# Kernel optimization log

Measured on AMD Instinct MI355X. Metric: run time of the kernel, lower is better.

## Reference

```python
import jax, jax.numpy as jnp
import numpy as np
import math

B, S, E = 4, 2048, 1024

def setup_inputs() -> dict:
    key = jax.random.key(0)
    ks = jax.random.split(key, 12)
    scale = 1.0 / math.sqrt(E)
    inp = {
        "query": jax.random.normal(ks[0], (B, S, E), jnp.float32),
        "key_": jax.random.normal(ks[1], (B, S, E), jnp.float32),
        "value": jax.random.normal(ks[2], (B, S, E), jnp.float32),
        # causal mask, broadcast over batch: 1 = keep, 0 = mask
        "mask": jnp.broadcast_to(jnp.tril(jnp.ones((S, S), jnp.int32)), (B, S, S)),
        "Wq": jax.random.uniform(ks[3], (E, E), jnp.float32, -scale, scale),
        "bq": jax.random.uniform(ks[4], (E,), jnp.float32, -scale, scale),
        "Wk": jax.random.uniform(ks[5], (E, E), jnp.float32, -scale, scale),
        "bk": jax.random.uniform(ks[6], (E,), jnp.float32, -scale, scale),
        "Wv": jax.random.uniform(ks[7], (E, E), jnp.float32, -scale, scale),
        "bv": jax.random.uniform(ks[8], (E,), jnp.float32, -scale, scale),
        "Wo": jax.random.uniform(ks[9], (E, E), jnp.float32, -scale, scale),
        "bo": jax.random.uniform(ks[10], (E,), jnp.float32, -scale, scale),
    }
    return inp

def reference(query, key_, value, mask, Wq, bq, Wk, bk, Wv, bv, Wo, bo):
    # Linear projections (torch Linear: x @ W.T + b)
    Q = jnp.einsum('bse,fe->bsf', query, Wq) + bq
    K = jnp.einsum('bse,fe->bsf', key_, Wk) + bk
    V = jnp.einsum('bse,fe->bsf', value, Wv) + bv
    # NOTE: module never splits heads; scores over full embed_dim, scaled by sqrt(embed_dim)
    scores = jnp.einsum('bqe,bke->bqk', Q, K) / jnp.sqrt(jnp.asarray(E, Q.dtype))
    scores = jnp.where(mask == 0, -jnp.inf, scores)
    attn = jax.nn.softmax(scores, axis=-1)
    attn_out = jnp.einsum('bqk,bke->bqe', attn, V)
    return jnp.einsum('bse,fe->bsf', attn_out, Wo) + bo
```

## Files before the change

### kernel.cpp

```cpp
#include <hip/hip_runtime.h>

typedef __bf16 bf16;
typedef __attribute__((ext_vector_type(8))) __bf16 bf16x8;
typedef __attribute__((ext_vector_type(4))) __bf16 bf16x4;
typedef __attribute__((ext_vector_type(2))) __bf16 bf16x2;
typedef __attribute__((ext_vector_type(4))) float f32x4;

#define DEVINL __device__ __forceinline__

DEVINL void gload_lds16(const bf16* g, bf16* l) {
    __builtin_amdgcn_global_load_lds(
        (__attribute__((address_space(1))) unsigned int*)(unsigned long long)g,
        (__attribute__((address_space(3))) unsigned int*)l,
        16, 0, 0);
}

DEVINL void xcd_swizzle(int& bx, int& by) {
    const int gx = gridDim.x, gy = gridDim.y;
    const int l = blockIdx.y * gx + blockIdx.x;
    const int xcd = l & 7;
    const int li = l >> 3;
    by = xcd * (gy >> 3) + li / gx;
    bx = li - (li / gx) * gx;
}

DEVINL void xcd_swizzle_bal(int& bx, int& by) {
    const int gx = gridDim.x, gy = gridDim.y;
    const int l = blockIdx.y * gx + blockIdx.x;
    const int xcd = l & 7;
    const int li = l >> 3;
    const int j = li / gx;
    bx = li - j * gx;
    by = j ? (gy - 1 - xcd) : xcd;
}

__global__ __launch_bounds__(256) void cvt4_f32_to_bf16(
    const float* __restrict__ a, const float* __restrict__ b,
    const float* __restrict__ c, const float* __restrict__ d,
    bf16* __restrict__ out, int n4) {
    int i = blockIdx.x * blockDim.x + threadIdx.x;
    if (i >= n4) return;
    const float* src = (blockIdx.z == 0) ? a : (blockIdx.z == 1) ? b
                     : (blockIdx.z == 2) ? c : d;
    bf16* dst = out + (size_t)blockIdx.z * (size_t)n4 * 4;
    float4 f = ((const float4*)src)[i];
    bf16x4 o;
    o.x = (bf16)f.x; o.y = (bf16)f.y; o.z = (bf16)f.z; o.w = (bf16)f.w;
    ((bf16x4*)dst)[i] = o;
}

__global__ __launch_bounds__(256) void transpose_bf16(
    const unsigned short* __restrict__ in, unsigned short* __restrict__ out,
    int R, int C) {
    __shared__ unsigned short t[64][65];
    const size_t bo = (size_t)blockIdx.z * R * C;
    const int r0 = blockIdx.y * 64, c0 = blockIdx.x * 64;
    const int tr = threadIdx.x >> 4;
    const int tc = threadIdx.x & 15;
#pragma unroll
    for (int i = 0; i < 4; i++) {
        int r = tr + i * 16;
        ushort4 v = *(const ushort4*)&in[bo + (size_t)(r0 + r) * C + (c0 + tc * 4)];
        t[r][tc * 4 + 0] = v.x; t[r][tc * 4 + 1] = v.y;
        t[r][tc * 4 + 2] = v.z; t[r][tc * 4 + 3] = v.w;
    }
    __syncthreads();
#pragma unroll
    for (int i = 0; i < 4; i++) {
        int r = tr + i * 16;
        ushort4 v;
        v.x = t[tc * 4 + 0][r]; v.y = t[tc * 4 + 1][r];
        v.z = t[tc * 4 + 2][r]; v.w = t[tc * 4 + 3][r];
        *(ushort4*)&out[bo + (size_t)(c0 + r) * R + (r0 + tc * 4)] = v;
    }
}

__global__ __launch_bounds__(256) void bias_fold(
    const float* __restrict__ Wo, const float* __restrict__ bv,
    const float* __restrict__ bo, float* __restrict__ bout) {
    const int e = blockIdx.x * 4 + (threadIdx.x >> 6);
    const int lane = threadIdx.x & 63;
    float s = 0.f;
    for (int k = lane; k < 1024; k += 64) s += Wo[e * 1024 + k] * bv[k];
#pragma unroll
    for (int off = 32; off > 0; off >>= 1) s += __shfl_xor(s, off, 64);
    if (lane == 0) bout[e] = s + bo[e];
}

__global__ __launch_bounds__(256) void gemm_bt128(
    const bf16* __restrict__ A, const bf16* __restrict__ B,
    bf16* __restrict__ C, int M, int N, int K) {
    int bx, by;
    xcd_swizzle(bx, by);
    const int m0 = by * 128, n0 = bx * 128;

    __shared__ __align__(16) bf16 As[2][128 * 32];
    __shared__ __align__(16) bf16 Bs[2][128 * 32];

    const int tid = threadIdx.x;
    const int wave = tid >> 6;
    const int lane = tid & 63;
    const int lr = lane & 15;
    const int lq = lane >> 4;
    const int wm = (wave >> 1) * 64;
    const int wn = (wave & 1) * 64;
    const int srow = lane >> 2;
    const int scol = ((lane & 3) ^ ((lane >> 3) & 3)) * 8;

    const bf16* gA = A + (size_t)(m0 + wave * 16 + srow) * K + scol;
    const bf16* gB = B + (size_t)(n0 + wave * 16 + srow) * K + scol;
    const size_t rowskip = (size_t)64 * K;
    const int rsw = (lq ^ ((lr >> 1) & 3)) * 8;

    f32x4 acc[4][4];
    const f32x4 fzero = {0.f, 0.f, 0.f, 0.f};
#pragma unroll
    for (int i = 0; i < 4; i++)
#pragma unroll
        for (int j = 0; j < 4; j++) acc[i][j] = fzero;

#define STAGE128(bufi)                                          \
    do {                                                        \
        gload_lds16(gA,           As[bufi] + wave * 512);       \
        gload_lds16(gA + rowskip, As[bufi] + (wave + 4) * 512); \
        gload_lds16(gB,           Bs[bufi] + wave * 512);       \
        gload_lds16(gB + rowskip, Bs[bufi] + (wave + 4) * 512); \
        gA += 32; gB += 32;                                     \
    } while (0)

    STAGE128(0);
    int cur = 0;
    for (int k0 = 0; k0 < K; k0 += 32) {
        __syncthreads();
        if (k0 + 32 < K) STAGE128(cur ^ 1);

        bf16x8 af[4], bfr[4];
#pragma unroll
        for (int i = 0; i < 4; i++)
            af[i] = *(const bf16x8*)(As[cur] + (wm + i * 16 + lr) * 32 + rsw);
#pragma unroll
        for (int j = 0; j < 4; j++)
            bfr[j] = *(const bf16x8*)(Bs[cur] + (wn + j * 16 + lr) * 32 + rsw);
#pragma unroll
        for (int i = 0; i < 4; i++)
#pragma unroll
            for (int j = 0; j < 4; j++)
                acc[i][j] = __builtin_amdgcn_mfma_f32_16x16x32_bf16(
                    af[i], bfr[j], acc[i][j], 0, 0, 0);
        cur ^= 1;
    }
#undef STAGE128

#pragma unroll
    for (int j = 0; j < 4; j++) {
        const int col = n0 + wn + j * 16 + lr;
#pragma unroll
        for (int i = 0; i < 4; i++) {
            const int rowb = m0 + wm + i * 16 + lq * 4;
#pragma unroll
            for (int r = 0; r < 4; r++)
                C[(size_t)(rowb + r) * N + col] = (bf16)acc[i][j][r];
        }
    }
}

__global__ __launch_bounds__(256) void gemm_projf(
    const float* __restrict__ A0, const float* __restrict__ A1,
    const float* __restrict__ A2, const bf16* __restrict__ Bw,
    const float* __restrict__ bias0, const float* __restrict__ bias1,
    bf16* __restrict__ Cq, int M, int N, int K) {
    int bx, by;
    xcd_swizzle(bx, by);
    const int bz = blockIdx.z;
    const int m0 = by * 128, n0 = bx * 128;

    const float* Af = (bz == 0) ? A0 : (bz == 1) ? A1 : A2;
    const bf16* B = Bw + (size_t)bz * (size_t)N * K;
    const float* bias = (bz == 0) ? bias0 : (bz == 1) ? bias1 : nullptr;
    bf16* C = Cq + (size_t)bz * (size_t)M * N;

    __shared__ __align__(16) bf16 As[2][128 * 32];
    __shared__ __align__(16) bf16 Bs[2][128 * 32];

    const int tid = threadIdx.x;
    const int wave = tid >> 6;
    const int lane = tid & 63;
    const int lr = lane & 15;
    const int lq = lane >> 4;
    const int wm = (wave >> 1) * 64;
    const int wn = (wave & 1) * 64;
    const int srow = lane >> 2;
    const int gsrc = (lane & 3) ^ ((lane >> 3) & 3);

    const float* fA = Af + (size_t)(m0 + wave * 16 + srow) * K + gsrc * 8;
    const bf16*  gB = B + (size_t)(n0 + wave * 16 + srow) * K + gsrc * 8;
    const size_t rsA = (size_t)64 * K;
    const size_t rsB = (size_t)64 * K;
    const int rsw = (lq ^ ((lr >> 1) & 3)) * 8;

    f32x4 acc[4][4];
    const f32x4 fzero = {0.f, 0.f, 0.f, 0.f};
#pragma unroll
    for (int i = 0; i < 4; i++)
#pragma unroll
        for (int j = 0; j < 4; j++) acc[i][j] = fzero;

#define STGP(bufi)                                                        \
    do {                                                                  \
        float4 a00 = *(const float4*)(fA);                                \
        float4 a01 = *(const float4*)(fA + 4);                            \
        float4 a10 = *(const float4*)(fA + rsA);                          \
        float4 a11 = *(const float4*)(fA + rsA + 4);                      \
        gload_lds16(gB,       Bs[bufi] + wave * 512);                     \
        gload_lds16(gB + rsB, Bs[bufi] + (wave + 4) * 512);               \
        bf16x8 p0, p1;                                                    \
        p0[0] = (bf16)a00.x; p0[1] = (bf16)a00.y;                         \
        p0[2] = (bf16)a00.z; p0[3] = (bf16)a00.w;                         \
        p0[4] = (bf16)a01.x; p0[5] = (bf16)a01.y;                         \
        p0[6] = (bf16)a01.z; p0[7] = (bf16)a01.w;                         \
        p1[0] = (bf16)a10.x; p1[1] = (bf16)a10.y;                         \
        p1[2] = (bf16)a10.z; p1[3] = (bf16)a10.w;                         \
        p1[4] = (bf16)a11.x; p1[5] = (bf16)a11.y;                         \
        p1[6] = (bf16)a11.z; p1[7] = (bf16)a11.w;                         \
        *(bf16x8*)(As[bufi] + wave * 512 + lane * 8) = p0;                \
        *(bf16x8*)(As[bufi] + (wave + 4) * 512 + lane * 8) = p1;          \
        fA += 32; gB += 32;                                               \
    } while (0)

    STGP(0);
    int cur = 0;
    for (int k0 = 0; k0 < K; k0 += 32) {
        __syncthreads();
        if (k0 + 32 < K) STGP(cur ^ 1);

        bf16x8 af[4], bfr[4];
#pragma unroll
        for (int i = 0; i < 4; i++)
            af[i] = *(const bf16x8*)(As[cur] + (wm + i * 16 + lr) * 32 + rsw);
#pragma unroll
        for (int j = 0; j < 4; j++)
            bfr[j] = *(const bf16x8*)(Bs[cur] + (wn + j * 16 + lr) * 32 + rsw);
#pragma unroll
        for (int i = 0; i < 4; i++)
#pragma unroll
            for (int j = 0; j < 4; j++)
                acc[i][j] = __builtin_amdgcn_mfma_f32_16x16x32_bf16(
                    af[i], bfr[j], acc[i][j], 0, 0, 0);
        cur ^= 1;
    }
#undef STGP

#pragma unroll
    for (int j = 0; j < 4; j++) {
        const int col = n0 + wn + j * 16 + lr;
        const float bb = bias ? bias[col] : 0.0f;
#pragma unroll
        for (int i = 0; i < 4; i++) {
            const int rowb = m0 + wm + i * 16 + lq * 4;
#pragma unroll
            for (int r = 0; r < 4; r++)
                C[(size_t)(rowb + r) * N + col] = (bf16)(acc[i][j][r] + bb);
        }
    }
}

__global__ __launch_bounds__(256) void gemm_sc(
    const bf16* __restrict__ Qb, const bf16* __restrict__ Kb,
    bf16* __restrict__ Sc, int S, int E) {
    int bx, by;
    xcd_swizzle_bal(bx, by);
    const int bz = blockIdx.z;
    const int m0 = by * 128, n0 = bx * 64;
    if (n0 > m0 + 127) return;

    const bf16* A = Qb + (size_t)bz * S * E;
    const bf16* B = Kb + (size_t)bz * S * E;

    __shared__ __align__(16) bf16 As[2][128 * 32];
    __shared__ __align__(16) bf16 Bs[2][64 * 32];

    const int tid = threadIdx.x;
    const int wave = tid >> 6;
    const int lane = tid & 63;
    const int lr = lane & 15;
    const int lq = lane >> 4;
    const int wm = wave * 32;
    const int srow = lane >> 2;
    const int scol = ((lane & 3) ^ ((lane >> 3) & 3)) * 8;

    const bf16* gA = A + (size_t)(m0 + wave * 16 + srow) * E + scol;
    const bf16* gB = B + (size_t)(n0 + wave * 16 + srow) * E + scol;
    const size_t rowskip = (size_t)64 * E;
    const int rsw = (lq ^ ((lr >> 1) & 3)) * 8;

    f32x4 acc[2][4];
    const f32x4 fzero = {0.f, 0.f, 0.f, 0.f};
#pragma unroll
    for (int i = 0; i < 2; i++)
#pragma unroll
        for (int j = 0; j < 4; j++) acc[i][j] = fzero;

#define STAGES(bufi)                                            \
    do {                                                        \
        gload_lds16(gA,           As[bufi] + wave * 512);       \
        gload_lds16(gA + rowskip, As[bufi] + (wave + 4) * 512); \
        gload_lds16(gB,           Bs[bufi] + wave * 512);       \
        gA += 32; gB += 32;                                     \
    } while (0)

    STAGES(0);
    int cur = 0;
    for (int k0 = 0; k0 < E; k0 += 32) {
        __syncthreads();
        if (k0 + 32 < E) STAGES(cur ^ 1);

        bf16x8 af[2], bfr[4];
#pragma unroll
        for (int i = 0; i < 2; i++)
            af[i] = *(const bf16x8*)(As[cur] + (wm + i * 16 + lr) * 32 + rsw);
#pragma unroll
        for (int j = 0; j < 4; j++)
            bfr[j] = *(const bf16x8*)(Bs[cur] + (j * 16 + lr) * 32 + rsw);
#pragma unroll
        for (int i = 0; i < 2; i++)
#pragma unroll
            for (int j = 0; j < 4; j++)
                acc[i][j] = __builtin_amdgcn_mfma_f32_16x16x32_bf16(
                    af[i], bfr[j], acc[i][j], 0, 0, 0);
        cur ^= 1;
    }
#undef STAGES

    bf16* dst = Sc + (size_t)bz * S * S;
#pragma unroll
    for (int j = 0; j < 4; j++) {
        const int col = n0 + j * 16 + lr;
#pragma unroll
        for (int i = 0; i < 2; i++) {
            const int rowb = m0 + wm + i * 16 + lq * 4;
#pragma unroll
            for (int r = 0; r < 4; r++)
                dst[(size_t)(rowb + r) * S + col] =
                    (bf16)(acc[i][j][r] * 0.03125f);
        }
    }
}

__global__ __launch_bounds__(256) void softmax_causal(
    const bf16* __restrict__ Sc, bf16* __restrict__ P, int S) {
    const int row = blockIdx.x;
    const int q = row & (S - 1);
    const bf16* src = Sc + (size_t)row * S;
    bf16* dst = P + (size_t)row * S;
    const int L = q + 1;
    const int tid = threadIdx.x;
    const int k0 = tid * 8;

    bf16x8 u = ((const bf16x8*)src)[tid];
    float v[8];
    float mx = -3.0e38f;
#pragma unroll
    for (int i = 0; i < 8; i++) {
        v[i] = (k0 + i < L) ? (float)u[i] : -3.0e38f;
        mx = fmaxf(mx, v[i]);
    }
#pragma unroll
    for (int off = 32; off > 0; off >>= 1) mx = fmaxf(mx, __shfl_xor(mx, off, 64));
    __shared__ float redm[4], reds[4];
    if ((tid & 63) == 0) redm[tid >> 6] = mx;
    __syncthreads();
    mx = fmaxf(fmaxf(redm[0], redm[1]), fmaxf(redm[2], redm[3]));

    float sum = 0.f;
#pragma unroll
    for (int i = 0; i < 8; i++) {
        float e = (v[i] > -1.0e38f) ? __expf(v[i] - mx) : 0.f;
        v[i] = e;
        sum += e;
    }
#pragma unroll
    for (int off = 32; off > 0; off >>= 1) sum += __shfl_xor(sum, off, 64);
    if ((tid & 63) == 0) reds[tid >> 6] = sum;
    __syncthreads();
    sum = reds[0] + reds[1] + reds[2] + reds[3];
    const float inv = 1.0f / sum;
    bf16x8 o;
#pragma unroll
    for (int i = 0; i < 8; i++) o[i] = (bf16)(v[i] * inv);
    ((bf16x8*)dst)[tid] = o;
}

__global__ __launch_bounds__(256, 2) void gemm_pv128(
    const bf16* __restrict__ A, const bf16* __restrict__ B,
    const float* __restrict__ bias, float* __restrict__ C,
    int M, int N, int K,
    long long sA, long long sB, long long sC,
    float scale) {
    int bx, by;
    xcd_swizzle_bal(bx, by);
    const int bz = blockIdx.z;
    const int m0 = by * 128, n0 = bx * 128;
    int Keff = m0 + 128; if (Keff > K) Keff = K;
    const int NT = Keff >> 5;

    A += (size_t)bz * sA;
    B += (size_t)bz * sB;

    __shared__ __align__(16) bf16 As[4][128 * 32];
    __shared__ __align__(16) bf16 Bs[4][128 * 32];

    const int tid = threadIdx.x;
    const int wave = tid >> 6;
    const int lane = tid & 63;
    const int lr = lane & 15;
    const int lq = lane >> 4;
    const int wm = (wave >> 1) * 64;
    const int wn = (wave & 1) * 64;

    const int srow = lane >> 2;
    const int scol = ((lane & 3) ^ ((lane >> 3) & 3)) * 8;
    const bf16* gA = A + (size_t)(m0 + wave * 16 + srow) * K + scol;
    const bf16* gB = B + (size_t)(n0 + wave * 16 + srow) * K + scol;
    const size_t rowskip = (size_t)64 * K;

    const int rsw = (lq ^ ((lr >> 1) & 3)) * 8;

    f32x4 acc[4][4];
    const f32x4 fzero = {0.f, 0.f, 0.f, 0.f};
#pragma unroll
    for (int i = 0; i < 4; i++)
#pragma unroll
        for (int j = 0; j < 4; j++) acc[i][j] = fzero;

#define STAGEV(bufi, koff)                                                 \
    do {                                                                   \
        gload_lds16(gA + (koff),           As[bufi] + wave * 512);         \
        gload_lds16(gA + rowskip + (koff), As[bufi] + (wave + 4) * 512);   \
        gload_lds16(gB + (koff),           Bs[bufi] + wave * 512);         \
        gload_lds16(gB + rowskip + (koff), Bs[bufi] + (wave + 4) * 512);   \
    } while (0)

    STAGEV(0, 0);
    STAGEV(1, 32);
    STAGEV(2, 64);
    asm volatile("s_waitcnt vmcnt(8)" ::: "memory");
    __builtin_amdgcn_s_barrier();

    for (int t = 0; t < NT; ++t) {
        const int bfi = t & 3;

        bf16x8 af[4], bfr[4];
#pragma unroll
        for (int i = 0; i < 4; i++)
            af[i] = *(const bf16x8*)(As[bfi] + (wm + i * 16 + lr) * 32 + rsw);
#pragma unroll
        for (int j = 0; j < 4; j++)
            bfr[j] = *(const bf16x8*)(Bs[bfi] + (wn + j * 16 + lr) * 32 + rsw);

        if (t + 3 < NT) STAGEV((t + 3) & 3, (t + 3) * 32);

        const int rem = NT - 1 - t;
        if (rem >= 3)      asm volatile("s_waitcnt vmcnt(8)" ::: "memory");
        else if (rem == 2) asm volatile("s_waitcnt vmcnt(4)" ::: "memory");
        else if (rem == 1) asm volatile("s_waitcnt vmcnt(0)" ::: "memory");
        __builtin_amdgcn_s_barrier();
        __builtin_amdgcn_sched_barrier(0);

        __builtin_amdgcn_s_setprio(1);
#pragma unroll
        for (int i = 0; i < 4; i++)
#pragma unroll
            for (int j = 0; j < 4; j++)
                acc[i][j] = __builtin_amdgcn_mfma_f32_16x16x32_bf16(
                    af[i], bfr[j], acc[i][j], 0, 0, 0);
        __builtin_amdgcn_s_setprio(0);
        __builtin_amdgcn_s_barrier();
    }
#undef STAGEV

#pragma unroll
    for (int j = 0; j < 4; j++) {
        const int col = n0 + wn + j * 16 + lr;
        const float bb = bias[col];
#pragma unroll
        for (int i = 0; i < 4; i++) {
            const int rowb = m0 + wm + i * 16 + lq * 4;
#pragma unroll
            for (int r = 0; r < 4; r++)
                C[(size_t)bz * sC + (size_t)(rowb + r) * N + col] =
                    acc[i][j][r] * scale + bb;
        }
    }
}

extern "C" void kernel_launch(void* const* d_in, const int* in_sizes, int n_in,
                              void* d_out, int out_size, void* d_ws, size_t ws_size,
                              hipStream_t stream) {
    const int B = 4, S = 2048, E = 1024;
    const size_t SBE = (size_t)B * S * E;
    const size_t EE = (size_t)E * E;
    const size_t BSS = (size_t)B * S * S;

    const float* q_in = (const float*)d_in[0];
    const float* k_in = (const float*)d_in[1];
    const float* v_in = (const float*)d_in[2];
    const float* Wq = (const float*)d_in[4];
    const float* bq = (const float*)d_in[5];
    const float* Wk = (const float*)d_in[6];
    const float* bk = (const float*)d_in[7];
    const float* Wv = (const float*)d_in[8];
    const float* bv = (const float*)d_in[9];
    const float* Wo = (const float*)d_in[10];
    const float* bo = (const float*)d_in[11];

    char* ws = (char*)d_ws;
    bf16* QKVb = (bf16*)ws;
    bf16* VWt  = (bf16*)(ws + 3 * SBE * 2);
    bf16* Sc   = (bf16*)(ws + 4 * SBE * 2);
    bf16* Pb   = (bf16*)(ws + 4 * SBE * 2 + BSS * 2);
    bf16* Wb   = (bf16*)(ws + 4 * SBE * 2 + 2 * BSS * 2);
    bf16* WvT  = Wb + 4 * EE;
    float* bout = (float*)(WvT + EE);

    bf16* Qb = QKVb;
    bf16* Kb = QKVb + SBE;
    bf16* VW = QKVb + 2 * SBE;
    bf16* Wob = Wb + 3 * EE;
    bf16* Wvo = Wb + 2 * EE;

    dim3 blk(256);

    dim3 gcvt4((int)(EE / 4 / 256), 1, 4);
    cvt4_f32_to_bf16<<<gcvt4, blk, 0, stream>>>(Wq, Wk, Wv, Wo, Wb, (int)(EE / 4));

    dim3 gtw(16, 16, 1);
    transpose_bf16<<<gtw, blk, 0, stream>>>((const unsigned short*)(Wb + 2 * EE),
                                            (unsigned short*)WvT, E, E);
    dim3 gwvo(E / 128, E / 128, 1);
    gemm_bt128<<<gwvo, blk, 0, stream>>>(Wob, WvT, Wvo, E, E, E);
    bias_fold<<<256, blk, 0, stream>>>(Wo, bv, bo, bout);

    dim3 gproj(E / 128, (B * S) / 128, 3);
    gemm_projf<<<gproj, blk, 0, stream>>>(q_in, k_in, v_in, Wb, bq, bk,
                                          QKVb, B * S, E, E);

    dim3 gt(E / 64, S / 64, B);
    transpose_bf16<<<gt, blk, 0, stream>>>((const unsigned short*)VW,
                                           (unsigned short*)VWt, S, E);

    dim3 gsc(S / 64, S / 128, B);
    gemm_sc<<<gsc, blk, 0, stream>>>(Qb, Kb, Sc, S, E);

    softmax_causal<<<B * S, blk, 0, stream>>>(Sc, Pb, S);

    dim3 gpv(E / 128, S / 128, B);
    gemm_pv128<<<gpv, blk, 0, stream>>>(Pb, VWt, bout, (float*)d_out, S, E, S,
                                        (long long)S * S, (long long)E * S,
                                        (long long)S * E, 1.f);
}
```

Before: 429.4 us.

## Software-pipeline fp32 A loads in projection GEMM and widen score tiles

The projection GEMM now issues the fp32 A-tile global loads two iterations ahead in registers, then converts and writes them to LDS after the fragment reads, with a single barrier at the end of each iteration. The goal is to hide global load latency behind the MFMA work. The score GEMM moves from 128x64 to 128x128 tiles, with each wave computing a 64x64 sub-tile. That gives more reuse per LDS load but makes causal tile skipping coarser and raises register pressure.

```diff
diff --git a/kernel.cpp b/kernel.cpp
--- a/kernel.cpp
+++ b/kernel.cpp
@@ -197,6 +197,7 @@
     const size_t rsA = (size_t)64 * K;
     const size_t rsB = (size_t)64 * K;
     const int rsw = (lq ^ ((lr >> 1) & 3)) * 8;
+    const int NT = K >> 5;
 
     f32x4 acc[4][4];
     const f32x4 fzero = {0.f, 0.f, 0.f, 0.f};
@@ -205,14 +206,18 @@
 #pragma unroll
         for (int j = 0; j < 4; j++) acc[i][j] = fzero;
 
-#define STGP(bufi)                                                        \
+    float4 a00, a01, a10, a11;
+
+#define LOADA(kt)                                                         \
     do {                                                                  \
-        float4 a00 = *(const float4*)(fA);                                \
-        float4 a01 = *(const float4*)(fA + 4);                            \
-        float4 a10 = *(const float4*)(fA + rsA);                          \
-        float4 a11 = *(const float4*)(fA + rsA + 4);                      \
-        gload_lds16(gB,       Bs[bufi] + wave * 512);                     \
-        gload_lds16(gB + rsB, Bs[bufi] + (wave + 4) * 512);               \
+        const float* p_ = fA + (size_t)(kt) * 32;                         \
+        a00 = *(const float4*)(p_);                                       \
+        a01 = *(const float4*)(p_ + 4);                                   \
+        a10 = *(const float4*)(p_ + rsA);                                 \
+        a11 = *(const float4*)(p_ + rsA + 4);                             \
+    } while (0)
+#define WRITEA(bufi)                                                      \
+    do {                                                                  \
         bf16x8 p0, p1;                                                    \
         p0[0] = (bf16)a00.x; p0[1] = (bf16)a00.y;                         \
         p0[2] = (bf16)a00.z; p0[3] = (bf16)a00.w;                         \
@@ -224,15 +229,21 @@
         p1[6] = (bf16)a11.z; p1[7] = (bf16)a11.w;                         \
         *(bf16x8*)(As[bufi] + wave * 512 + lane * 8) = p0;                \
         *(bf16x8*)(As[bufi] + (wave + 4) * 512 + lane * 8) = p1;          \
-        fA += 32; gB += 32;                                               \
     } while (0)
-
-    STGP(0);
+#define STAGEB(bufi, kt)                                                  \
+    do {                                                                  \
+        gload_lds16(gB + (size_t)(kt) * 32,       Bs[bufi] + wave * 512); \
+        gload_lds16(gB + rsB + (size_t)(kt) * 32, Bs[bufi] + (wave + 4) * 512); \
+    } while (0)
+
+    LOADA(0);
+    STAGEB(0, 0);
+    WRITEA(0);
+    LOADA(1);
+    __syncthreads();
+
     int cur = 0;
-    for (int k0 = 0; k0 < K; k0 += 32) {
-        __syncthreads();
-        if (k0 + 32 < K) STGP(cur ^ 1);
-
+    for (int t = 0; t < NT; ++t) {
         bf16x8 af[4], bfr[4];
 #pragma unroll
         for (int i = 0; i < 4; i++)
@@ -240,15 +251,25 @@
 #pragma unroll
         for (int j = 0; j < 4; j++)
             bfr[j] = *(const bf16x8*)(Bs[cur] + (wn + j * 16 + lr) * 32 + rsw);
+
+        if (t + 1 < NT) {
+            WRITEA(cur ^ 1);
+            STAGEB(cur ^ 1, t + 1);
+            if (t + 2 < NT) LOADA(t + 2);
+        }
+
 #pragma unroll
         for (int i = 0; i < 4; i++)
 #pragma unroll
             for (int j = 0; j < 4; j++)
                 acc[i][j] = __builtin_amdgcn_mfma_f32_16x16x32_bf16(
                     af[i], bfr[j], acc[i][j], 0, 0, 0);
+        __syncthreads();
         cur ^= 1;
     }
-#undef STGP
+#undef LOADA
+#undef WRITEA
+#undef STAGEB
 
 #pragma unroll
     for (int j = 0; j < 4; j++) {
@@ -264,27 +285,28 @@
     }
 }
 
-__global__ __launch_bounds__(256) void gemm_sc(
+__global__ __launch_bounds__(256) void gemm_sc128(
     const bf16* __restrict__ Qb, const bf16* __restrict__ Kb,
     bf16* __restrict__ Sc, int S, int E) {
     int bx, by;
     xcd_swizzle_bal(bx, by);
     const int bz = blockIdx.z;
-    const int m0 = by * 128, n0 = bx * 64;
+    const int m0 = by * 128, n0 = bx * 128;
     if (n0 > m0 + 127) return;
 
     const bf16* A = Qb + (size_t)bz * S * E;
     const bf16* B = Kb + (size_t)bz * S * E;
 
     __shared__ __align__(16) bf16 As[2][128 * 32];
-    __shared__ __align__(16) bf16 Bs[2][64 * 32];
+    __shared__ __align__(16) bf16 Bs[2][128 * 32];
 
     const int tid = threadIdx.x;
     const int wave = tid >> 6;
     const int lane = tid & 63;
     const int lr = lane & 15;
     const int lq = lane >> 4;
-    const int wm = wave * 32;
+    const int wm = (wave >> 1) * 64;
+    const int wn = (wave & 1) * 64;
     const int srow = lane >> 2;
     const int scol = ((lane & 3) ^ ((lane >> 3) & 3)) * 8;
 
@@ -293,50 +315,51 @@
     const size_t rowskip = (size_t)64 * E;
     const int rsw = (lq ^ ((lr >> 1) & 3)) * 8;
 
-    f32x4 acc[2][4];
+    f32x4 acc[4][4];
     const f32x4 fzero = {0.f, 0.f, 0.f, 0.f};
 #pragma unroll
-    for (int i = 0; i < 2; i++)
+    for (int i = 0; i < 4; i++)
 #pragma unroll
         for (int j = 0; j < 4; j++) acc[i][j] = fzero;
 
-#define STAGES(bufi)                                            \
+#define STAGESC(bufi)                                           \
     do {                                                        \
         gload_lds16(gA,           As[bufi] + wave * 512);       \
         gload_lds16(gA + rowskip, As[bufi] + (wave + 4) * 512); \
         gload_lds16(gB,           Bs[bufi] + wave * 512);       \
+        gload_lds16(gB + rowskip, Bs[bufi] + (wave + 4) * 512); \
         gA += 32; gB += 32;                                     \
     } while (0)
 
-    STAGES(0);
+    STAGESC(0);
     int cur = 0;
     for (int k0 = 0; k0 < E; k0 += 32) {
         __syncthreads();
-        if (k0 + 32 < E) STAGES(cur ^ 1);
-
-        bf16x8 af[2], bfr[4];
-#pragma unroll
-        for (int i = 0; i < 2; i++)
+        if (k0 + 32 < E) STAGESC(cur ^ 1);
+
+        bf16x8 af[4], bfr[4];
+#pragma unroll
+        for (int i = 0; i < 4; i++)
             af[i] = *(const bf16x8*)(As[cur] + (wm + i * 16 + lr) * 32 + rsw);
 #pragma unroll
         for (int j = 0; j < 4; j++)
-            bfr[j] = *(const bf16x8*)(Bs[cur] + (j * 16 + lr) * 32 + rsw);
-#pragma unroll
-        for (int i = 0; i < 2; i++)
+            bfr[j] = *(const bf16x8*)(Bs[cur] + (wn + j * 16 + lr) * 32 + rsw);
+#pragma unroll
+        for (int i = 0; i < 4; i++)
 #pragma unroll
             for (int j = 0; j < 4; j++)
                 acc[i][j] = __builtin_amdgcn_mfma_f32_16x16x32_bf16(
                     af[i], bfr[j], acc[i][j], 0, 0, 0);
         cur ^= 1;
     }
-#undef STAGES
+#undef STAGESC
 
     bf16* dst = Sc + (size_t)bz * S * S;
 #pragma unroll
     for (int j = 0; j < 4; j++) {
-        const int col = n0 + j * 16 + lr;
-#pragma unroll
-        for (int i = 0; i < 2; i++) {
+        const int col = n0 + wn + j * 16 + lr;
+#pragma unroll
+        for (int i = 0; i < 4; i++) {
             const int rowb = m0 + wm + i * 16 + lq * 4;
 #pragma unroll
             for (int r = 0; r < 4; r++)
@@ -548,8 +571,8 @@
     transpose_bf16<<<gt, blk, 0, stream>>>((const unsigned short*)VW,
                                            (unsigned short*)VWt, S, E);
 
-    dim3 gsc(S / 64, S / 128, B);
-    gemm_sc<<<gsc, blk, 0, stream>>>(Qb, Kb, Sc, S, E);
+    dim3 gsc(S / 128, S / 128, B);
+    gemm_sc128<<<gsc, blk, 0, stream>>>(Qb, Kb, Sc, S, E);
 
     softmax_causal<<<B * S, blk, 0, stream>>>(Sc, Pb, S);
 
```

After: 398.8 us. -7.1%, faster.
